# Performance work log

Measured on AMD Instinct MI355X. Metric: run time of the kernel, lower is better.

Reference implementation:

```python
import jax, jax.numpy as jnp
import numpy as np

N_NODES = 50000
N_EDGES = 800000
NFEAT, NHID, NCLASS = 512, 128, 16


def _with_self_loops(edge_idx, n):
    loop = jnp.arange(n, dtype=edge_idx.dtype)
    src = jnp.concatenate([edge_idx[0], loop])  # [E+N]
    dst = jnp.concatenate([edge_idx[1], loop])
    return src, dst


def gcn_conv(x, src, dst, W, b, n):
    # GCNConv with add aggregation, self-loops, symmetric normalization.
    h = x @ W  # [N, out]
    ones = jnp.ones(src.shape[0], dtype=h.dtype)
    deg = jax.ops.segment_sum(ones, dst, num_segments=n)  # in-degree incl. self-loops
    dinv = jnp.where(deg > 0, jax.lax.rsqrt(deg), 0.0)
    norm = dinv[src] * dinv[dst]  # [E+N]
    msg = h[src] * norm[:, None]  # gather + scale
    out = jax.ops.segment_sum(msg, dst, num_segments=n)  # scatter-add
    return out + b


def setup_inputs() -> dict:
    key = jax.random.key(0)
    ks = jax.random.split(key, 8)
    x = jax.random.normal(ks[0], (N_NODES, NFEAT), dtype=jnp.float32)
    edge_idx = jax.random.randint(ks[1], (2, N_EDGES), 0, N_NODES, dtype=jnp.int64)
    s1 = 1.0 / np.sqrt(NFEAT)
    s2 = 1.0 / np.sqrt(NHID)
    W1 = jax.random.uniform(ks[2], (NFEAT, NHID), jnp.float32, -s1, s1)
    b1 = jnp.zeros((NHID,), jnp.float32)
    W2 = jax.random.uniform(ks[3], (NHID, NHID), jnp.float32, -s2, s2)
    b2 = jnp.zeros((NHID,), jnp.float32)
    Wc = jax.random.uniform(ks[4], (NHID, NCLASS), jnp.float32, -s2, s2)
    bc = jax.random.uniform(ks[5], (NCLASS,), jnp.float32, -s2, s2)
    return {"x": x, "edge_idx": edge_idx, "W1": W1, "b1": b1, "W2": W2, "b2": b2, "Wc": Wc, "bc": bc}


def reference(x, edge_idx, W1, b1, W2, b2, Wc, bc):
    n = x.shape[0]
    src, dst = _with_self_loops(edge_idx, n)
    h = gcn_conv(x, src, dst, W1, b1, n)
    h = jax.nn.relu(h)  # dropout is identity in eval mode
    h = gcn_conv(h, src, dst, W2, b2, n)
    h = jax.nn.relu(h)
    logits = h @ Wc + bc
    return jax.nn.log_softmax(logits, axis=1)
```

## Files before the change

### kernel.cpp

```cpp
#include <hip/hip_runtime.h>
#include <math.h>

#define NFEAT 512
#define NHID  128
#define NCLASS 16
#define SCAN_BS 512
#define AGG_BLOCKS 2048

typedef __attribute__((ext_vector_type(8))) short short8;
typedef __attribute__((ext_vector_type(4))) float f32x4;

static __device__ __forceinline__ ushort f2b(float f) {
    union { float f; uint u; } v; v.f = f;
    uint r = v.u + 0x7FFFu + ((v.u >> 16) & 1u);
    return (ushort)(r >> 16);
}
static __device__ __forceinline__ float b2f_lo(uint bits) {
    union { uint u; float f; } v; v.u = bits << 16; return v.f;
}
static __device__ __forceinline__ float b2f_hi(uint bits) {
    union { uint u; float f; } v; v.u = bits & 0xffff0000u; return v.f;
}


__global__ void k_init_deg(int* __restrict__ deg, int n) {
    int i = blockIdx.x * blockDim.x + threadIdx.x;
    if (i < n) deg[i] = 1;
}

__global__ void k_count(const int* __restrict__ dst, int e, int* __restrict__ deg) {
    int i = blockIdx.x * blockDim.x + threadIdx.x;
    if (i < e) atomicAdd(&deg[dst[i]], 1);
}

__global__ void k_dinv(const int* __restrict__ deg, float* __restrict__ dinv,
                       int* __restrict__ gcnt, int* __restrict__ cursor, int n) {
    int i = blockIdx.x * blockDim.x + threadIdx.x;
    if (i < n) {
        dinv[i] = rsqrtf((float)deg[i]);
        gcnt[i] = (deg[i] + 7) >> 3;
        cursor[i] = 0;
    }
}

__global__ void k_scan1(const int* __restrict__ in, int* __restrict__ offs,
                        int* __restrict__ bsum, int n) {
    __shared__ int s[SCAN_BS];
    int t = threadIdx.x;
    int i = blockIdx.x * SCAN_BS + t;
    int v = (i < n) ? in[i] : 0;
    s[t] = v;
    for (int off = 1; off < SCAN_BS; off <<= 1) {
        __syncthreads();
        int x = (t >= off) ? s[t - off] : 0;
        __syncthreads();
        s[t] += x;
    }
    __syncthreads();
    if (i < n) offs[i] = s[t] - v;
    if (t == SCAN_BS - 1) bsum[blockIdx.x] = s[t];
}

__global__ void k_scan2(int* __restrict__ bsum, int* __restrict__ offs, int nb, int n) {
    if (threadIdx.x == 0 && blockIdx.x == 0) {
        int run = 0;
        for (int b = 0; b < nb; b++) { int x = bsum[b]; bsum[b] = run; run += x; }
        offs[n] = run;
    }
}

__global__ void k_scan3(int* __restrict__ offs, const int* __restrict__ bsum, int n) {
    int i = blockIdx.x * SCAN_BS + threadIdx.x;
    if (i < n) offs[i] += bsum[blockIdx.x];
}

__global__ void k_fill_edges(const int* __restrict__ src, const int* __restrict__ dst, int e,
                             const int* __restrict__ goffs, int* __restrict__ cursor,
                             uint* __restrict__ colp32) {
    int i = blockIdx.x * blockDim.x + threadIdx.x;
    if (i < e) {
        int d = dst[i];
        int p = atomicAdd(&cursor[d], 1);
        colp32[(size_t)goffs[d] * 8 + p] = (uint)src[i];
    }
}

__global__ void k_fill_tail(const int* __restrict__ goffs, const int* __restrict__ deg,
                            uint* __restrict__ colp32, ushort* __restrict__ hs, int n) {
    int i = blockIdx.x * blockDim.x + threadIdx.x;
    if (i < 128) {
        int s = i >> 5, f = i & 31;
        hs[((size_t)s * (n + 1) + n) * 32 + f] = 0;
    }
    if (i < n) {
        int g0 = goffs[i], g1 = goffs[i + 1];
        size_t base = (size_t)g0 * 8;
        int d = deg[i];
        int slots = (g1 - g0) * 8;
        colp32[base + d - 1] = (uint)i;
        for (int p = d; p < slots; p++) colp32[base + p] = (uint)n;
        uint meta = (uint)(i + 1) << 16;
        for (int k = slots - 8; k < slots; k++) colp32[base + k] |= meta;
        if (i == 0) {
            int G = goffs[n];
            for (int k = 0; k < 32; k++) colp32[(size_t)G * 8 + k] = (uint)n;
        }
    }
}

__global__ void k_rankstart(const uint* __restrict__ colp32, const int* __restrict__ goffs,
                            int* __restrict__ rankgs, int n) {
    int r = blockIdx.x * blockDim.x + threadIdx.x;
    if (r >= AGG_BLOCKS) return;
    int G = goffs[n];
    int run = (G + AGG_BLOCKS - 1) / AGG_BLOCKS;
    int g = r * run;
    int ge = g + run; if (ge > G) ge = G;
    if (g >= G) { rankgs[r] = -1; return; }
    if (g > 0) {
        while (g < ge && !(colp32[(size_t)(g - 1) * 8] >> 16)) g++;
        if (g >= ge) { rankgs[r] = -1; return; }
    }
    rankgs[r] = g;
}


__global__ void k_tcast(const float* __restrict__ W1, const float* __restrict__ W2,
                        ushort* __restrict__ W1T, ushort* __restrict__ W2T) {
    int idx = blockIdx.x * 256 + threadIdx.x;
    if (idx < NFEAT * 128) {
        int k = idx >> 7, c = idx & 127;
        W1T[(size_t)c * NFEAT + k] = f2b(W1[idx]);
    } else {
        int j = idx - NFEAT * 128;
        if (j < NHID * 128) {
            int k = j >> 7, c = j & 127;
            W2T[(size_t)c * NHID + k] = f2b(W2[j]);
        }
    }
}


template<int A_F32>
__global__ __launch_bounds__(256) void k_gemm(const void* __restrict__ Aptr,
                                              const ushort* __restrict__ WT,
                                              const float* __restrict__ rowscale,
                                              ushort* __restrict__ Hs, int M, int K) {
    __shared__ ushort As[128][40];
    __shared__ ushort Bs[128][40];

    const int tid = threadIdx.x;
    const int wid = tid >> 6, lane = tid & 63;
    const int wr = wid >> 1, wc = wid & 1;
    const int lr = lane & 15, lk = (lane >> 4) * 8;
    const int rowbase = blockIdx.x * 128;

    f32x4 acc[4][4];
#pragma unroll
    for (int i = 0; i < 4; i++)
#pragma unroll
        for (int j = 0; j < 4; j++) acc[i][j] = (f32x4)0.f;

    const int sr = tid >> 1;
    const int sh = (tid & 1) * 16;

    for (int k0 = 0; k0 < K; k0 += 32) {
        {
            int gr = rowbase + sr;
            ushort tmp[16];
            if (A_F32) {
                const float* A = (const float*)Aptr;
                if (gr < M) {
                    const float* p = A + (size_t)gr * K + k0 + sh;
#pragma unroll
                    for (int q = 0; q < 4; q++) {
                        float4 v = *(const float4*)(p + q * 4);
                        tmp[q * 4 + 0] = f2b(v.x); tmp[q * 4 + 1] = f2b(v.y);
                        tmp[q * 4 + 2] = f2b(v.z); tmp[q * 4 + 3] = f2b(v.w);
                    }
                } else {
#pragma unroll
                    for (int q = 0; q < 16; q++) tmp[q] = 0;
                }
            } else {
                const ushort* A = (const ushort*)Aptr;
                if (gr < M) {
                    const ushort* p = A + (size_t)gr * K + k0 + sh;
                    *(short8*)&tmp[0] = *(const short8*)(p);
                    *(short8*)&tmp[8] = *(const short8*)(p + 8);
                } else {
#pragma unroll
                    for (int q = 0; q < 16; q++) tmp[q] = 0;
                }
            }
            *(short8*)&As[sr][sh]     = *(short8*)&tmp[0];
            *(short8*)&As[sr][sh + 8] = *(short8*)&tmp[8];
        }
        {
#pragma unroll
            for (int t = 0; t < 2; t++) {
                int c = tid + t * 256;
                int row = c >> 2, q = c & 3;
                short8 v = *(const short8*)(WT + (size_t)row * K + k0 + q * 8);
                *(short8*)&Bs[row][q * 8] = v;
            }
        }
        __syncthreads();

        short8 af[4], bfv[4];
#pragma unroll
        for (int i = 0; i < 4; i++) af[i] = *(const short8*)&As[wr * 64 + i * 16 + lr][lk];
#pragma unroll
        for (int j = 0; j < 4; j++) bfv[j] = *(const short8*)&Bs[wc * 64 + j * 16 + lr][lk];
#pragma unroll
        for (int i = 0; i < 4; i++)
#pragma unroll
            for (int j = 0; j < 4; j++)
                acc[i][j] = __builtin_amdgcn_mfma_f32_16x16x32_bf16(af[i], bfv[j], acc[i][j], 0, 0, 0);
        __syncthreads();
    }

#pragma unroll
    for (int i = 0; i < 4; i++) {
#pragma unroll
        for (int r = 0; r < 4; r++) {
            int row = rowbase + wr * 64 + i * 16 + (lane >> 4) * 4 + r;
            if (row < M) {
                float sc = rowscale[row];
#pragma unroll
                for (int j = 0; j < 4; j++) {
                    int slice = wc * 2 + (j >> 1);
                    int f = (j & 1) * 16 + lr;
                    Hs[((size_t)slice * (M + 1) + row) * 32 + f] = f2b(acc[i][j][r] * sc);
                }
            }
        }
    }
}


__global__ __launch_bounds__(256) void k_aggs(const ushort* __restrict__ hs,
                                              const uint* __restrict__ colp32,
                                              const int* __restrict__ rankgs,
                                              const int* __restrict__ goffs,
                                              const float* __restrict__ dinv,
                                              const float* __restrict__ bias,
                                              ushort* __restrict__ outp, int n) {
    const int b = blockIdx.x;
    const int s = (b & 7) >> 1;
    const int wid = threadIdx.x >> 6, lane = threadIdx.x & 63;
    const int e8 = lane >> 3, q = lane & 7;

    const int G = goffs[n];
    const int rank = ((b >> 3) * 2 + (b & 1)) * 4 + wid;
    const int run = (G + AGG_BLOCKS - 1) / AGG_BLOCKS;
    int gs = rankgs[rank];
    int ge = (rank + 1) * run; if (ge > G) ge = G;
    if (gs < 0 || gs >= ge) return;

    const ushort* hsl = hs + (size_t)s * (n + 1) * 32;
    const float4 bv = *(const float4*)(bias + s * 32 + q * 4);

    int g = gs;
    const uint* cp = colp32 + (size_t)g * 8 + e8;
    uint cw0 = cp[0], cw1 = cp[8], cw2 = cp[16];
    uint2 pk0 = *(const uint2*)(hsl + (size_t)(cw0 & 0xffffu) * 32 + q * 4);
    uint2 pk1 = *(const uint2*)(hsl + (size_t)(cw1 & 0xffffu) * 32 + q * 4);
    float fdv0 = (cw0 >> 16) ? dinv[(cw0 >> 16) - 1] : 0.f;
    float fdv1 = (cw1 >> 16) ? dinv[(cw1 >> 16) - 1] : 0.f;
    float a0 = 0.f, a1 = 0.f, a2 = 0.f, a3 = 0.f;

    while (true) {
        uint cw3 = cp[24];
        uint2 pk2 = *(const uint2*)(hsl + (size_t)(cw2 & 0xffffu) * 32 + q * 4);
        float fdv2 = (cw2 >> 16) ? dinv[(cw2 >> 16) - 1] : 0.f;

        a0 += b2f_lo(pk0.x); a1 += b2f_hi(pk0.x);
        a2 += b2f_lo(pk0.y); a3 += b2f_hi(pk0.y);

        if (cw0 >> 16) {
            int v = (int)(cw0 >> 16) - 1;
            float r0 = a0, r1 = a1, r2 = a2, r3 = a3;
#pragma unroll
            for (int off = 8; off <= 32; off <<= 1) {
                r0 += __shfl_xor(r0, off); r1 += __shfl_xor(r1, off);
                r2 += __shfl_xor(r2, off); r3 += __shfl_xor(r3, off);
            }
            r0 = fmaxf(fmaf(r0, fdv0, bv.x), 0.f);
            r1 = fmaxf(fmaf(r1, fdv0, bv.y), 0.f);
            r2 = fmaxf(fmaf(r2, fdv0, bv.z), 0.f);
            r3 = fmaxf(fmaf(r3, fdv0, bv.w), 0.f);
            if (lane < 8) {
                uint2 u;
                u.x = (uint)f2b(r0) | ((uint)f2b(r1) << 16);
                u.y = (uint)f2b(r2) | ((uint)f2b(r3) << 16);
                *(uint2*)(outp + (size_t)v * 128 + s * 32 + q * 4) = u;
            }
            if (g + 1 >= ge) break;
            a0 = a1 = a2 = a3 = 0.f;
        }
        g++; cp += 8;
        cw0 = cw1; cw1 = cw2; cw2 = cw3;
        pk0 = pk1; pk1 = pk2;
        fdv0 = fdv1; fdv1 = fdv2;
    }
}


__global__ __launch_bounds__(256) void k_classify(const ushort* __restrict__ h,
                                                  const float* __restrict__ Wc,
                                                  const float* __restrict__ bc,
                                                  float* __restrict__ out, int n) {
    __shared__ float Ws[128 * 16];
    int tid = threadIdx.x;
#pragma unroll
    for (int t = 0; t < 8; t++) Ws[tid + 256 * t] = Wc[tid + 256 * t];
    __syncthreads();

    int wid = tid >> 6, lane = tid & 63;
    int v = blockIdx.x * 4 + wid;
    if (v >= n) return;

    int j = lane & 15, c = lane >> 4;
    const ushort* hv = h + (size_t)v * 128 + c * 32;
    float acc = 0.f;
#pragma unroll
    for (int t = 0; t < 16; t++) {
        uint pk = *(const uint*)(hv + t * 2);
        acc = fmaf(b2f_lo(pk), Ws[(c * 32 + t * 2 + 0) * 16 + j], acc);
        acc = fmaf(b2f_hi(pk), Ws[(c * 32 + t * 2 + 1) * 16 + j], acc);
    }
    acc += __shfl_xor(acc, 16);
    acc += __shfl_xor(acc, 32);
    acc += bc[j];

    float m = acc;
#pragma unroll
    for (int o = 8; o >= 1; o >>= 1) m = fmaxf(m, __shfl_xor(m, o));
    float sum = expf(acc - m);
#pragma unroll
    for (int o = 8; o >= 1; o >>= 1) sum += __shfl_xor(sum, o);
    if (lane < 16) out[(size_t)v * 16 + j] = acc - m - logf(sum);
}


extern "C" void kernel_launch(void* const* d_in, const int* in_sizes, int n_in,
                              void* d_out, int out_size, void* d_ws, size_t ws_size,
                              hipStream_t stream) {
    const float* x  = (const float*)d_in[0];
    const int* eidx = (const int*)d_in[1];
    const float* W1 = (const float*)d_in[2];
    const float* b1 = (const float*)d_in[3];
    const float* W2 = (const float*)d_in[4];
    const float* b2 = (const float*)d_in[5];
    const float* Wc = (const float*)d_in[6];
    const float* bc = (const float*)d_in[7];
    float* out = (float*)d_out;

    const int N = in_sizes[0] / NFEAT;
    const int E = in_sizes[1] / 2;
    const int* src = eidx;
    const int* dst = eidx + E;

    char* p = (char*)d_ws;
    auto alloc = [&](size_t bytes) { char* r = p; p += (bytes + 255) & ~(size_t)255; return r; };
    int*    deg    = (int*)   alloc((size_t)N * 4);
    float*  dinv   = (float*) alloc((size_t)N * 4);
    int*    gcnt   = (int*)   alloc((size_t)N * 4);
    int*    goffs  = (int*)   alloc((size_t)(N + 1) * 4);
    int*    cursor = (int*)   alloc((size_t)N * 4);
    uint*   colp32 = (uint*)  alloc(((size_t)E + 8ull * N + 32) * 4);
    int*    rankgs = (int*)   alloc((size_t)AGG_BLOCKS * 4);
    int*    bsum   = (int*)   alloc((size_t)256 * 4);
    ushort* W1T    = (ushort*)alloc((size_t)128 * NFEAT * 2);
    ushort* W2T    = (ushort*)alloc((size_t)128 * NHID * 2);
    ushort* hs     = (ushort*)alloc((size_t)(N + 1) * NHID * 2);
    ushort* g1     = (ushort*)alloc((size_t)N * NHID * 2);
    ushort* g2     = (ushort*)alloc((size_t)N * NHID * 2);

    const int nb = (N + SCAN_BS - 1) / SCAN_BS;

    k_init_deg<<<(N + 255) / 256, 256, 0, stream>>>(deg, N);
    k_count<<<(E + 255) / 256, 256, 0, stream>>>(dst, E, deg);
    k_dinv<<<(N + 255) / 256, 256, 0, stream>>>(deg, dinv, gcnt, cursor, N);
    k_scan1<<<nb, SCAN_BS, 0, stream>>>(gcnt, goffs, bsum, N);
    k_scan2<<<1, 64, 0, stream>>>(bsum, goffs, nb, N);
    k_scan3<<<nb, SCAN_BS, 0, stream>>>(goffs, bsum, N);
    k_fill_edges<<<(E + 255) / 256, 256, 0, stream>>>(src, dst, E, goffs, cursor, colp32);
    k_fill_tail<<<(N + 255) / 256, 256, 0, stream>>>(goffs, deg, colp32, hs, N);
    k_rankstart<<<(AGG_BLOCKS + 255) / 256, 256, 0, stream>>>(colp32, goffs, rankgs, N);

    k_tcast<<<((NFEAT + NHID) * 128 + 255) / 256, 256, 0, stream>>>(W1, W2, W1T, W2T);

    const int gblocks = (N + 127) / 128;
    k_gemm<1><<<gblocks, 256, 0, stream>>>(x, W1T, dinv, hs, N, NFEAT);
    k_aggs<<<AGG_BLOCKS, 256, 0, stream>>>(hs, colp32, rankgs, goffs, dinv, b1, g1, N);
    k_gemm<0><<<gblocks, 256, 0, stream>>>(g1, W2T, dinv, hs, N, NHID);
    k_aggs<<<AGG_BLOCKS, 256, 0, stream>>>(hs, colp32, rankgs, goffs, dinv, b2, g2, N);
    k_classify<<<(N + 3) / 4, 256, 0, stream>>>(g2, Wc, bc, out, N);
}
```

Baseline: 266.6 us.

## Fuse setup kernels, parallelize block scan, shrink GEMM tile, deepen aggregation prefetch

Merges degree init with the weight transpose-cast, and folds dinv/cursor/group-count computation into the first scan kernel, which drops launches and the gcnt buffer. The serial block-sum scan is replaced by a wavefront shuffle scan. The GEMM tile shrinks from 128 to 64 rows with each wave covering a 32-column slice, doubling the block count for better occupancy on 50k rows at the cost of more reloads of the weight tile. The aggregation loop prefetches one more edge group ahead, with the padding at the end of the column array extended to match.

```diff
diff --git a/kernel.cpp b/kernel.cpp
--- a/kernel.cpp
+++ b/kernel.cpp
@@ -23,9 +23,21 @@
 }
 
 
-__global__ void k_init_deg(int* __restrict__ deg, int n) {
-    int i = blockIdx.x * blockDim.x + threadIdx.x;
-    if (i < n) deg[i] = 1;
+__global__ void k_init_tcast(const float* __restrict__ W1, const float* __restrict__ W2,
+                             ushort* __restrict__ W1T, ushort* __restrict__ W2T,
+                             int* __restrict__ deg, int n) {
+    int idx = blockIdx.x * 256 + threadIdx.x;
+    if (idx < n) deg[idx] = 1;
+    if (idx < NFEAT * 128) {
+        int k = idx >> 7, c = idx & 127;
+        W1T[(size_t)c * NFEAT + k] = f2b(W1[idx]);
+    } else {
+        int j = idx - NFEAT * 128;
+        if (j < NHID * 128) {
+            int k = j >> 7, c = j & 127;
+            W2T[(size_t)c * NHID + k] = f2b(W2[j]);
+        }
+    }
 }
 
 __global__ void k_count(const int* __restrict__ dst, int e, int* __restrict__ deg) {
@@ -33,22 +45,15 @@
     if (i < e) atomicAdd(&deg[dst[i]], 1);
 }
 
-__global__ void k_dinv(const int* __restrict__ deg, float* __restrict__ dinv,
-                       int* __restrict__ gcnt, int* __restrict__ cursor, int n) {
-    int i = blockIdx.x * blockDim.x + threadIdx.x;
-    if (i < n) {
-        dinv[i] = rsqrtf((float)deg[i]);
-        gcnt[i] = (deg[i] + 7) >> 3;
-        cursor[i] = 0;
-    }
-}
-
-__global__ void k_scan1(const int* __restrict__ in, int* __restrict__ offs,
+__global__ void k_scan1(const int* __restrict__ deg, float* __restrict__ dinv,
+                        int* __restrict__ cursor, int* __restrict__ offs,
                         int* __restrict__ bsum, int n) {
     __shared__ int s[SCAN_BS];
     int t = threadIdx.x;
     int i = blockIdx.x * SCAN_BS + t;
-    int v = (i < n) ? in[i] : 0;
+    int d = (i < n) ? deg[i] : 0;
+    if (i < n) { dinv[i] = rsqrtf((float)d); cursor[i] = 0; }
+    int v = (i < n) ? ((d + 7) >> 3) : 0;
     s[t] = v;
     for (int off = 1; off < SCAN_BS; off <<= 1) {
         __syncthreads();
@@ -62,11 +67,20 @@
 }
 
 __global__ void k_scan2(int* __restrict__ bsum, int* __restrict__ offs, int nb, int n) {
-    if (threadIdx.x == 0 && blockIdx.x == 0) {
-        int run = 0;
-        for (int b = 0; b < nb; b++) { int x = bsum[b]; bsum[b] = run; run += x; }
-        offs[n] = run;
-    }
+    int lane = threadIdx.x;
+    int carry = 0;
+    for (int base = 0; base < nb; base += 64) {
+        int i = base + lane;
+        int v = (i < nb) ? bsum[i] : 0;
+        int orig = v;
+        for (int off = 1; off < 64; off <<= 1) {
+            int t = __shfl_up(v, off);
+            if (lane >= off) v += t;
+        }
+        if (i < nb) bsum[i] = carry + v - orig;
+        carry += __shfl(v, 63);
+    }
+    if (lane == 0) offs[n] = carry;
 }
 
 __global__ void k_scan3(int* __restrict__ offs, const int* __restrict__ bsum, int n) {
@@ -103,7 +117,7 @@
         for (int k = slots - 8; k < slots; k++) colp32[base + k] |= meta;
         if (i == 0) {
             int G = goffs[n];
-            for (int k = 0; k < 32; k++) colp32[(size_t)G * 8 + k] = (uint)n;
+            for (int k = 0; k < 48; k++) colp32[(size_t)G * 8 + k] = (uint)n;
         }
     }
 }
@@ -125,76 +139,56 @@
 }
 
 
-__global__ void k_tcast(const float* __restrict__ W1, const float* __restrict__ W2,
-                        ushort* __restrict__ W1T, ushort* __restrict__ W2T) {
-    int idx = blockIdx.x * 256 + threadIdx.x;
-    if (idx < NFEAT * 128) {
-        int k = idx >> 7, c = idx & 127;
-        W1T[(size_t)c * NFEAT + k] = f2b(W1[idx]);
-    } else {
-        int j = idx - NFEAT * 128;
-        if (j < NHID * 128) {
-            int k = j >> 7, c = j & 127;
-            W2T[(size_t)c * NHID + k] = f2b(W2[j]);
-        }
-    }
-}
-
-
 template<int A_F32>
 __global__ __launch_bounds__(256) void k_gemm(const void* __restrict__ Aptr,
                                               const ushort* __restrict__ WT,
                                               const float* __restrict__ rowscale,
                                               ushort* __restrict__ Hs, int M, int K) {
-    __shared__ ushort As[128][40];
+    __shared__ ushort As[64][40];
     __shared__ ushort Bs[128][40];
 
     const int tid = threadIdx.x;
-    const int wid = tid >> 6, lane = tid & 63;
-    const int wr = wid >> 1, wc = wid & 1;
+    const int wc = tid >> 6, lane = tid & 63;
     const int lr = lane & 15, lk = (lane >> 4) * 8;
-    const int rowbase = blockIdx.x * 128;
-
-    f32x4 acc[4][4];
+    const int rowbase = blockIdx.x * 64;
+
+    f32x4 acc[4][2];
 #pragma unroll
     for (int i = 0; i < 4; i++)
 #pragma unroll
-        for (int j = 0; j < 4; j++) acc[i][j] = (f32x4)0.f;
-
-    const int sr = tid >> 1;
-    const int sh = (tid & 1) * 16;
+        for (int j = 0; j < 2; j++) acc[i][j] = (f32x4)0.f;
+
+    const int sr = tid >> 2;
+    const int sh = (tid & 3) * 8;
 
     for (int k0 = 0; k0 < K; k0 += 32) {
         {
             int gr = rowbase + sr;
-            ushort tmp[16];
+            ushort tmp[8];
             if (A_F32) {
                 const float* A = (const float*)Aptr;
                 if (gr < M) {
                     const float* p = A + (size_t)gr * K + k0 + sh;
 #pragma unroll
-                    for (int q = 0; q < 4; q++) {
+                    for (int q = 0; q < 2; q++) {
                         float4 v = *(const float4*)(p + q * 4);
                         tmp[q * 4 + 0] = f2b(v.x); tmp[q * 4 + 1] = f2b(v.y);
                         tmp[q * 4 + 2] = f2b(v.z); tmp[q * 4 + 3] = f2b(v.w);
                     }
                 } else {
 #pragma unroll
-                    for (int q = 0; q < 16; q++) tmp[q] = 0;
+                    for (int q = 0; q < 8; q++) tmp[q] = 0;
                 }
             } else {
                 const ushort* A = (const ushort*)Aptr;
                 if (gr < M) {
-                    const ushort* p = A + (size_t)gr * K + k0 + sh;
-                    *(short8*)&tmp[0] = *(const short8*)(p);
-                    *(short8*)&tmp[8] = *(const short8*)(p + 8);
+                    *(short8*)&tmp[0] = *(const short8*)(A + (size_t)gr * K + k0 + sh);
                 } else {
 #pragma unroll
-                    for (int q = 0; q < 16; q++) tmp[q] = 0;
+                    for (int q = 0; q < 8; q++) tmp[q] = 0;
                 }
             }
-            *(short8*)&As[sr][sh]     = *(short8*)&tmp[0];
-            *(short8*)&As[sr][sh + 8] = *(short8*)&tmp[8];
+            *(short8*)&As[sr][sh] = *(short8*)&tmp[0];
         }
         {
 #pragma unroll
@@ -207,15 +201,15 @@
         }
         __syncthreads();
 
-        short8 af[4], bfv[4];
-#pragma unroll
-        for (int i = 0; i < 4; i++) af[i] = *(const short8*)&As[wr * 64 + i * 16 + lr][lk];
-#pragma unroll
-        for (int j = 0; j < 4; j++) bfv[j] = *(const short8*)&Bs[wc * 64 + j * 16 + lr][lk];
+        short8 af[4], bfv[2];
+#pragma unroll
+        for (int i = 0; i < 4; i++) af[i] = *(const short8*)&As[i * 16 + lr][lk];
+#pragma unroll
+        for (int j = 0; j < 2; j++) bfv[j] = *(const short8*)&Bs[wc * 32 + j * 16 + lr][lk];
 #pragma unroll
         for (int i = 0; i < 4; i++)
 #pragma unroll
-            for (int j = 0; j < 4; j++)
+            for (int j = 0; j < 2; j++)
                 acc[i][j] = __builtin_amdgcn_mfma_f32_16x16x32_bf16(af[i], bfv[j], acc[i][j], 0, 0, 0);
         __syncthreads();
     }
@@ -224,14 +218,13 @@
     for (int i = 0; i < 4; i++) {
 #pragma unroll
         for (int r = 0; r < 4; r++) {
-            int row = rowbase + wr * 64 + i * 16 + (lane >> 4) * 4 + r;
+            int row = rowbase + i * 16 + (lane >> 4) * 4 + r;
             if (row < M) {
                 float sc = rowscale[row];
 #pragma unroll
-                for (int j = 0; j < 4; j++) {
-                    int slice = wc * 2 + (j >> 1);
-                    int f = (j & 1) * 16 + lr;
-                    Hs[((size_t)slice * (M + 1) + row) * 32 + f] = f2b(acc[i][j][r] * sc);
+                for (int j = 0; j < 2; j++) {
+                    int f = j * 16 + lr;
+                    Hs[((size_t)wc * (M + 1) + row) * 32 + f] = f2b(acc[i][j][r] * sc);
                 }
             }
         }
@@ -263,17 +256,19 @@
 
     int g = gs;
     const uint* cp = colp32 + (size_t)g * 8 + e8;
-    uint cw0 = cp[0], cw1 = cp[8], cw2 = cp[16];
+    uint cw0 = cp[0], cw1 = cp[8], cw2 = cp[16], cw3 = cp[24];
     uint2 pk0 = *(const uint2*)(hsl + (size_t)(cw0 & 0xffffu) * 32 + q * 4);
     uint2 pk1 = *(const uint2*)(hsl + (size_t)(cw1 & 0xffffu) * 32 + q * 4);
+    uint2 pk2 = *(const uint2*)(hsl + (size_t)(cw2 & 0xffffu) * 32 + q * 4);
     float fdv0 = (cw0 >> 16) ? dinv[(cw0 >> 16) - 1] : 0.f;
     float fdv1 = (cw1 >> 16) ? dinv[(cw1 >> 16) - 1] : 0.f;
+    float fdv2 = (cw2 >> 16) ? dinv[(cw2 >> 16) - 1] : 0.f;
     float a0 = 0.f, a1 = 0.f, a2 = 0.f, a3 = 0.f;
 
     while (true) {
-        uint cw3 = cp[24];
-        uint2 pk2 = *(const uint2*)(hsl + (size_t)(cw2 & 0xffffu) * 32 + q * 4);
-        float fdv2 = (cw2 >> 16) ? dinv[(cw2 >> 16) - 1] : 0.f;
+        uint cw4 = cp[32];
+        uint2 pk3 = *(const uint2*)(hsl + (size_t)(cw3 & 0xffffu) * 32 + q * 4);
+        float fdv3 = (cw3 >> 16) ? dinv[(cw3 >> 16) - 1] : 0.f;
 
         a0 += b2f_lo(pk0.x); a1 += b2f_hi(pk0.x);
         a2 += b2f_lo(pk0.y); a3 += b2f_hi(pk0.y);
@@ -300,9 +295,9 @@
             a0 = a1 = a2 = a3 = 0.f;
         }
         g++; cp += 8;
-        cw0 = cw1; cw1 = cw2; cw2 = cw3;
-        pk0 = pk1; pk1 = pk2;
-        fdv0 = fdv1; fdv1 = fdv2;
+        cw0 = cw1; cw1 = cw2; cw2 = cw3; cw3 = cw4;
+        pk0 = pk1; pk1 = pk2; pk2 = pk3;
+        fdv0 = fdv1; fdv1 = fdv2; fdv2 = fdv3;
     }
 }
 
@@ -366,10 +361,9 @@
     auto alloc = [&](size_t bytes) { char* r = p; p += (bytes + 255) & ~(size_t)255; return r; };
     int*    deg    = (int*)   alloc((size_t)N * 4);
     float*  dinv   = (float*) alloc((size_t)N * 4);
-    int*    gcnt   = (int*)   alloc((size_t)N * 4);
     int*    goffs  = (int*)   alloc((size_t)(N + 1) * 4);
     int*    cursor = (int*)   alloc((size_t)N * 4);
-    uint*   colp32 = (uint*)  alloc(((size_t)E + 8ull * N + 32) * 4);
+    uint*   colp32 = (uint*)  alloc(((size_t)E + 8ull * N + 64) * 4);
     int*    rankgs = (int*)   alloc((size_t)AGG_BLOCKS * 4);
     int*    bsum   = (int*)   alloc((size_t)256 * 4);
     ushort* W1T    = (ushort*)alloc((size_t)128 * NFEAT * 2);
@@ -380,19 +374,16 @@
 
     const int nb = (N + SCAN_BS - 1) / SCAN_BS;
 
-    k_init_deg<<<(N + 255) / 256, 256, 0, stream>>>(deg, N);
+    k_init_tcast<<<((NFEAT + NHID) * 128 + 255) / 256, 256, 0, stream>>>(W1, W2, W1T, W2T, deg, N);
     k_count<<<(E + 255) / 256, 256, 0, stream>>>(dst, E, deg);
-    k_dinv<<<(N + 255) / 256, 256, 0, stream>>>(deg, dinv, gcnt, cursor, N);
-    k_scan1<<<nb, SCAN_BS, 0, stream>>>(gcnt, goffs, bsum, N);
+    k_scan1<<<nb, SCAN_BS, 0, stream>>>(deg, dinv, cursor, goffs, bsum, N);
     k_scan2<<<1, 64, 0, stream>>>(bsum, goffs, nb, N);
     k_scan3<<<nb, SCAN_BS, 0, stream>>>(goffs, bsum, N);
     k_fill_edges<<<(E + 255) / 256, 256, 0, stream>>>(src, dst, E, goffs, cursor, colp32);
     k_fill_tail<<<(N + 255) / 256, 256, 0, stream>>>(goffs, deg, colp32, hs, N);
     k_rankstart<<<(AGG_BLOCKS + 255) / 256, 256, 0, stream>>>(colp32, goffs, rankgs, N);
 
-    k_tcast<<<((NFEAT + NHID) * 128 + 255) / 256, 256, 0, stream>>>(W1, W2, W1T, W2T);
-
-    const int gblocks = (N + 127) / 128;
+    const int gblocks = (N + 63) / 64;
     k_gemm<1><<<gblocks, 256, 0, stream>>>(x, W1T, dinv, hs, N, NFEAT);
     k_aggs<<<AGG_BLOCKS, 256, 0, stream>>>(hs, colp32, rankgs, goffs, dinv, b1, g1, N);
     k_gemm<0><<<gblocks, 256, 0, stream>>>(g1, W2T, dinv, hs, N, NHID);
```

Result: no change. 261.6 us (-1.9%).
